# Performance work log

Hardware: AMD Instinct MI355X
Metric: run time of the kernel (lower is better)

The kernel has to match this reference:

```python
import jax, jax.numpy as jnp
import numpy as np

EPS = 1e-6          # module eps for denominator
KERNEL_EPS = 1e-4   # performer softmax_kernel numerical eps


def softmax_kernel(data, projection):
    # data: [n, l, h, e]; projection: [m, e] -> features [n, l, h, m]
    d = data.shape[-1]
    m = projection.shape[0]
    data_normalizer = d ** -0.25
    ratio = m ** -0.5
    data_dash = jnp.einsum('nlhe,me->nlhm', data * data_normalizer, projection)
    diag_data = (0.5 * (data_normalizer ** 2)) * jnp.sum(data * data, axis=-1, keepdims=True)
    # numerically stable exp with per-row max subtraction
    data_dash = ratio * (jnp.exp(data_dash - diag_data - jnp.max(data_dash, axis=-1, keepdims=True)) + KERNEL_EPS)
    return data_dash


def _gaussian_orthogonal_random_matrix(nb_rows, nb_cols, seed=0):
    rng = np.random.default_rng(seed)
    blocks = []
    for _ in range(int(np.ceil(nb_rows / nb_cols))):
        q, _ = np.linalg.qr(rng.standard_normal((nb_cols, nb_cols)))
        blocks.append(q.T)
    proj = np.concatenate(blocks, axis=0)[:nb_rows]
    # scaling=0: chi-distributed row multipliers
    multiplier = np.linalg.norm(rng.standard_normal((nb_rows, nb_cols)), axis=1)
    return (multiplier[:, None] * proj).astype(np.float32)


def setup_inputs() -> dict:
    n, l, h, e = 2, 2048, 8, 64
    nb_features = l  # module: nb_features = l when l >= e
    key = jax.random.key(0)
    kq, kk, kv = jax.random.split(key, 3)
    queries = jax.random.normal(kq, (n, l, h, e), jnp.float32)
    keys = jax.random.normal(kk, (n, l, h, e), jnp.float32)
    values = jax.random.normal(kv, (n, l, h, e), jnp.float32)
    projection = jnp.asarray(_gaussian_orthogonal_random_matrix(nb_features, e))
    return {"queries": queries, "keys": keys, "values": values, "projection": projection}


def reference(queries, keys, values, projection):
    # Performer linear attention, batched (bi=None) branch
    q = softmax_kernel(queries, projection)   # [n, l, h, m]
    k = softmax_kernel(keys, projection)      # [n, l, h, m]
    kv = jnp.einsum('nshm,nshe->nhem', k, values)              # [n, h, e, m]
    z = 1.0 / (jnp.einsum('nlhm,nhm->nlh', q, k.sum(axis=1)) + EPS)  # [n, l, h]
    v = jnp.einsum('nlhm,nhem,nlh->nlhe', q, kv, z)             # [n, l, h, e]
    return v
```

## Files before the change

### kernel.cpp

```cpp
#include <hip/hip_runtime.h>


#define LL 2048
#define HH 8
#define MM 2048
#define ROWSTR 512

#define NORMC 0.35355339059327373f
#define LOG2E 1.4426950408889634f
#define NORMC2 (NORMC * LOG2E)
#define RATIO 0.022097086912079608f
#define KEPS 1e-4f
#define REPS (RATIO * KEPS)
#define EPSD 1e-6f

#define KVSPLIT 2097152
#define RSPLIT 32768

typedef __attribute__((ext_vector_type(8))) short short8;
typedef __attribute__((ext_vector_type(16))) float f32x16;

#define MFMA32(a, b, c) __builtin_amdgcn_mfma_f32_32x32x16_bf16((a), (b), (c), 0, 0, 0)

__device__ __forceinline__ void wg_barrier_lds() {
    asm volatile("s_waitcnt lgkmcnt(0)" ::: "memory");
    __builtin_amdgcn_s_barrier();
    __builtin_amdgcn_sched_barrier(0);
}

__device__ __forceinline__ f32x16 zero16() {
    f32x16 v;
    #pragma unroll
    for (int i = 0; i < 16; ++i) v[i] = 0.f;
    return v;
}
__device__ __forceinline__ unsigned short f2bf(float f) {
    union { float f; unsigned int u; } v; v.f = f;
    unsigned int r = v.u + 0x7fffu + ((v.u >> 16) & 1u);
    return (unsigned short)(r >> 16);
}
__device__ __forceinline__ unsigned int pk2(float lo, float hi) {
    return __builtin_amdgcn_perm(__float_as_uint(hi), __float_as_uint(lo), 0x07060302u);
}
__device__ __forceinline__ float bf2f(unsigned short u) {
    union { unsigned int ui; float f; } v; v.ui = ((unsigned int)u) << 16; return v.f;
}

template <bool BF16>
__device__ __forceinline__ short8 row_load8(const void* src, size_t rowbase, int off) {
    if (BF16) {
        return *(const short8*)((const unsigned short*)src + rowbase + off);
    } else {
        const float* p = (const float*)src + rowbase + off;
        float4 f0 = ((const float4*)p)[0], f1 = ((const float4*)p)[1];
        union { unsigned int u[4]; short8 s; } v;
        v.u[0] = pk2(f0.x, f0.y); v.u[1] = pk2(f0.z, f0.w);
        v.u[2] = pk2(f1.x, f1.y); v.u[3] = pk2(f1.z, f1.w);
        return v.s;
    }
}

template <bool BF16>
__device__ __forceinline__ void tile_load(const void* src, size_t base, size_t rstride,
                                          int t, uint4& A, uint4& B) {
    const int row = t >> 2, c16 = (t & 3) * 16;
    if (BF16) {
        const unsigned short* p = (const unsigned short*)src + base + (size_t)row * rstride + c16;
        A = *(const uint4*)p;
        B = *(const uint4*)(p + 8);
    } else {
        const float* p = (const float*)src + base + (size_t)row * rstride + c16;
        float4 f0 = ((const float4*)p)[0], f1 = ((const float4*)p)[1];
        float4 f2 = ((const float4*)p)[2], f3 = ((const float4*)p)[3];
        A.x = pk2(f0.x, f0.y); A.y = pk2(f0.z, f0.w);
        A.z = pk2(f1.x, f1.y); A.w = pk2(f1.z, f1.w);
        B.x = pk2(f2.x, f2.y); B.y = pk2(f2.z, f2.w);
        B.z = pk2(f3.x, f3.y); B.w = pk2(f3.z, f3.w);
    }
}
__device__ __forceinline__ void tile_store72(unsigned short* D, int t, uint4 A, uint4 B) {
    const int row = t >> 2, c16 = (t & 3) * 16;
    *(uint4*)&D[row * 72 + c16] = A;
    *(uint4*)&D[row * 72 + c16 + 8] = B;
}

template <bool BF16>
__device__ __forceinline__ void vt_load(const void* V, size_t base, int t, uint4& A, uint4& B) {
    const int s0 = (t & 31) * 2, e0 = (t >> 5) * 8;
    if (BF16) {
        const unsigned short* p = (const unsigned short*)V + base + (size_t)s0 * ROWSTR + e0;
        A = *(const uint4*)p;
        B = *(const uint4*)(p + ROWSTR);
    } else {
        const float* p = (const float*)V + base + (size_t)s0 * ROWSTR + e0;
        float4 f0 = ((const float4*)p)[0], f1 = ((const float4*)p)[1];
        const float* q = p + ROWSTR;
        float4 g0 = ((const float4*)q)[0], g1 = ((const float4*)q)[1];
        A.x = pk2(f0.x, f0.y); A.y = pk2(f0.z, f0.w);
        A.z = pk2(f1.x, f1.y); A.w = pk2(f1.z, f1.w);
        B.x = pk2(g0.x, g0.y); B.y = pk2(g0.z, g0.w);
        B.z = pk2(g1.x, g1.y); B.w = pk2(g1.z, g1.w);
    }
}
__device__ __forceinline__ void vt_store72(unsigned short* VT, int t, uint4 A, uint4 B) {
    const int s0 = (t & 31) * 2, e0 = (t >> 5) * 8;
    const unsigned ua[4] = {A.x, A.y, A.z, A.w}, ub[4] = {B.x, B.y, B.z, B.w};
    #pragma unroll
    for (int i = 0; i < 4; ++i) {
        *(unsigned*)&VT[(e0 + 2 * i) * 72 + s0] = (ua[i] & 0xFFFFu) | (ub[i] << 16);
        *(unsigned*)&VT[(e0 + 2 * i + 1) * 72 + s0] = (ua[i] >> 16) | (ub[i] & 0xFFFF0000u);
    }
}

__device__ __forceinline__ short8 xfrag(const unsigned int pd[8], int cp, int hi) {
    const unsigned int s0 = hi ? pd[4 * cp + 0] : pd[4 * cp + 2];
    const unsigned int s1 = hi ? pd[4 * cp + 1] : pd[4 * cp + 3];
    const unsigned int r0 = (unsigned int)__shfl_xor((int)s0, 32);
    const unsigned int r1 = (unsigned int)__shfl_xor((int)s1, 32);
    union { unsigned int u[4]; short8 s; } v;
    v.u[0] = hi ? r0 : pd[4 * cp + 0];
    v.u[1] = hi ? r1 : pd[4 * cp + 1];
    v.u[2] = hi ? pd[4 * cp + 2] : r0;
    v.u[3] = hi ? pd[4 * cp + 3] : r1;
    return v.s;
}

__global__ void LinearAttention_15985868276494_detect(const unsigned short* __restrict__ P,
                                                      float* __restrict__ flag) {
    if (threadIdx.x == 0) {
        int sane = 1;
        #pragma unroll
        for (int i = 0; i < 16; ++i) {
            const unsigned e = (P[2 * i] >> 7) & 0xFF;
            if (e < 101 || e > 141) sane = 0;
        }
        *flag = sane ? 1.0f : 0.0f;
    }
}

template <bool BF16>
__device__ void stats_impl(const void* X, const void* P, float* cws,
                           unsigned short* Ps, float* red) {
    const int t = threadIdx.x;
    const int w = t >> 6, ln = t & 31, hi = (t >> 5) & 1;
    const int mstrip = w & 1, rstrip = w >> 1;
    const int row_base = blockIdx.x * 256;

    short8 xb[4];
    #pragma unroll
    for (int c = 0; c < 4; ++c)
        xb[c] = row_load8<BF16>(X, (size_t)(row_base + rstrip * 32 + ln) * 64, 16 * c + 8 * hi);

    const bool stP = (t < 256);
    const int tl = t & 255;
    uint4 pA, pB;
    if (stP) {
        uint4 a0, b0;
        tile_load<BF16>(P, 0, 64, tl, a0, b0);
        tile_store72(Ps, tl, a0, b0);
        tile_load<BF16>(P, (size_t)64 * 64, 64, tl, pA, pB);
    }
    wg_barrier_lds();

    float rmax = -3e38f;
    for (int i = 0; i < 32; ++i) {
        const int cur = i & 1;
        unsigned short* Pc = Ps + cur * 4608;
        f32x16 acc = zero16();
        #pragma unroll
        for (int c = 0; c < 4; ++c) {
            const short8 af = *(const short8*)&Pc[(32 * mstrip + ln) * 72 + 16 * c + 8 * hi];
            acc = MFMA32(af, xb[c], acc);
        }
        if (stP && i + 1 < 32) {
            tile_store72(Ps + (cur ^ 1) * 4608, tl, pA, pB);
            if (i + 2 < 32)
                tile_load<BF16>(P, (size_t)((i + 2) * 64) * 64, 64, tl, pA, pB);
        }
        #pragma unroll
        for (int r = 0; r < 16; ++r) rmax = fmaxf(rmax, acc[r]);
        wg_barrier_lds();
    }
    rmax = fmaxf(rmax, __shfl_xor(rmax, 32));
    if (hi == 0) red[w * 32 + ln] = rmax;
    float s2 = 0.f;
    if (mstrip == 0) {
        #pragma unroll
        for (int c = 0; c < 4; ++c) {
            union { short8 s; unsigned int u[4]; } uv; uv.s = xb[c];
            #pragma unroll
            for (int i2 = 0; i2 < 4; ++i2) {
                const float lo = bf2f((unsigned short)(uv.u[i2] & 0xFFFF));
                const float hv = bf2f((unsigned short)(uv.u[i2] >> 16));
                s2 = fmaf(lo, lo, s2); s2 = fmaf(hv, hv, s2);
            }
        }
        s2 += __shfl_xor(s2, 32);
    }
    wg_barrier_lds();
    if (mstrip == 0 && hi == 0) {
        const float rm = fmaxf(red[w * 32 + ln], red[(w + 1) * 32 + ln]);
        const int rg = row_base + rstrip * 32 + ln;
        const int n = rg >> 14, l = (rg >> 3) & 2047, h = rg & 7;
        cws[(size_t)((n << 3) | h) * LL + l] =
            (NORMC * rm + (0.5f * NORMC * NORMC) * s2) * LOG2E;
    }
}

__global__ __launch_bounds__(1024, 4) void LinearAttention_15985868276494_stats(
        const void* K, const void* Q, const void* P, const float* flag,
        float* c_k, float* c_q) {
    __shared__ unsigned short Ps[2 * 64 * 72];
    __shared__ float red[512];
    const void* X = (blockIdx.y == 0) ? K : Q;
    float* cws = (blockIdx.y == 0) ? c_k : c_q;
    if (*flag != 0.f) stats_impl<true>(X, P, cws, Ps, red);
    else stats_impl<false>(X, P, cws, Ps, red);
}

template <bool BF16>
__device__ void kv_impl(const void* K, const void* V, const void* P, const float* cws,
                        float* kvf01, float* ksum01, char* smem) {
    unsigned short* Ks = (unsigned short*)smem;
    unsigned short* VT = (unsigned short*)(smem + 18432);
    float* cks = (float*)(smem + 36864);
    float* fin = (float*)smem;

    const int t = threadIdx.x;
    const int w = t >> 6, ln = t & 31, hi = (t >> 5) & 1;
    const int w2 = w & 3, ep = w >> 2;
    const int sstrip = w2 & 1, msub = w2 >> 1;
    const int mc = ep * 2 + msub;
    const int bid = blockIdx.x;
    const int xcd = bid & 7, rr = bid >> 3;
    const int gq = rr >> 3, mtb = rr & 7;
    const int g = gq * 8 + xcd;
    const int nh = g >> 1, sp = g & 1;
    const int n = nh >> 3, h = nh & 7;
    const size_t xbase = (size_t)n * (LL * ROWSTR) + (size_t)h * 64;
    const int st0 = sp * 16;
    const int mbase = mtb * 256;

    const bool stK = (t < 256), stV = (t >= 256 && t < 512);
    const int tl = t & 255;

    short8 pb[4];
    #pragma unroll
    for (int c = 0; c < 4; ++c)
        pb[c] = row_load8<BF16>(P, (size_t)(mbase + mc * 32 + ln) * 64, 16 * c + 8 * hi);

    uint4 kA, kB, vA, vB; float ckr = 0.f;
    if (stK) {
        tile_load<BF16>(K, xbase + (size_t)(st0 * 64) * ROWSTR, ROWSTR, tl, kA, kB);
        tile_store72(Ks, tl, kA, kB);
        tile_load<BF16>(K, xbase + (size_t)((st0 + 1) * 64) * ROWSTR, ROWSTR, tl, kA, kB);
    } else if (stV) {
        vt_load<BF16>(V, xbase + (size_t)(st0 * 64) * ROWSTR, tl, vA, vB);
        vt_store72(VT, tl, vA, vB);
        vt_load<BF16>(V, xbase + (size_t)((st0 + 1) * 64) * ROWSTR, tl, vA, vB);
    }
    if (t < 64) {
        cks[t] = cws[(size_t)nh * LL + st0 * 64 + t];
        ckr = cws[(size_t)nh * LL + (st0 + 1) * 64 + t];
    }
    wg_barrier_lds();

    const short8 ones = {0x3F80, 0x3F80, 0x3F80, 0x3F80, 0x3F80, 0x3F80, 0x3F80, 0x3F80};
    f32x16 akv0 = zero16(), akv1 = zero16(), aks = zero16();

    for (int i = 0; i < 16; ++i) {
        const int cur = i & 1;
        unsigned short* Kc = Ks + cur * 4608;
        unsigned short* Vc = VT + cur * 4608;
        const float* cc = cks + cur * 64;
        f32x16 D = zero16();
        #pragma unroll
        for (int c = 0; c < 4; ++c) {
            const short8 af = *(const short8*)&Kc[(32 * sstrip + ln) * 72 + 16 * c + 8 * hi];
            D = MFMA32(af, pb[c], D);
        }
        if (i + 1 < 16) {
            if (stK) tile_store72(Ks + (cur ^ 1) * 4608, tl, kA, kB);
            else if (stV) vt_store72(VT + (cur ^ 1) * 4608, tl, vA, vB);
            if (t < 64) cks[(cur ^ 1) * 64 + t] = ckr;
            if (i + 2 < 16) {
                const int st = st0 + i + 2;
                if (stK) tile_load<BF16>(K, xbase + (size_t)(st * 64) * ROWSTR, ROWSTR, tl, kA, kB);
                else if (stV) vt_load<BF16>(V, xbase + (size_t)(st * 64) * ROWSTR, tl, vA, vB);
                if (t < 64) ckr = cws[(size_t)nh * LL + st * 64 + t];
            }
        }
        unsigned int pd[8];
        #pragma unroll
        for (int gIdx = 0; gIdx < 4; ++gIdx) {
            const float4 c4 = *(const float4*)&cc[32 * sstrip + 8 * gIdx + 4 * hi];
            const float ca[4] = {c4.x, c4.y, c4.z, c4.w};
            float f[4];
            #pragma unroll
            for (int b = 0; b < 4; ++b) {
                const float arg = fminf(fmaf(D[4 * gIdx + b], NORMC2, -ca[b]), 0.f);
                f[b] = fmaf(__builtin_amdgcn_exp2f(arg), RATIO, REPS);
            }
            pd[2 * gIdx] = pk2(f[0], f[1]);
            pd[2 * gIdx + 1] = pk2(f[2], f[3]);
        }
        #pragma unroll
        for (int cp = 0; cp < 2; ++cp) {
            const short8 bf = xfrag(pd, cp, hi);
            const int scol = 32 * sstrip + 16 * cp + 8 * hi;
            const short8 v0 = *(const short8*)&Vc[ln * 72 + scol];
            const short8 v1 = *(const short8*)&Vc[(32 + ln) * 72 + scol];
            akv0 = MFMA32(v0, bf, akv0);
            akv1 = MFMA32(v1, bf, akv1);
            aks = MFMA32(ones, bf, aks);
        }
        wg_barrier_lds();
    }
    #pragma unroll 1
    for (int e4 = 0; e4 < 4; ++e4) {
        if (ep == e4) {
            const int slot = (w2 * 64 + (t & 63)) * 33;
            #pragma unroll
            for (int r = 0; r < 16; ++r) fin[slot + r] = akv0[r];
            #pragma unroll
            for (int r = 0; r < 16; ++r) fin[slot + 16 + r] = akv1[r];
            fin[slot + 32] = aks[0];
        }
        wg_barrier_lds();
        if (ep == e4) {
            const int tt = t & 255;
            const int mt = mtb * 4 + e4;
            const int e = tt >> 2;
            const int t16 = e >> 5, e5 = e & 31;
            const int hi_s = (e5 >> 2) & 1;
            const int reg = 16 * t16 + (e5 & 3) + 4 * (e5 >> 3);
            float* dst = kvf01 + (size_t)sp * KVSPLIT + (size_t)nh * (64 * MM)
                       + (size_t)e * MM + mt * 64 + (tt & 3) * 16;
            #pragma unroll
            for (int jq = 0; jq < 4; ++jq) {
                float o[4];
                #pragma unroll
                for (int b = 0; b < 4; ++b) {
                    const int m_local = (tt & 3) * 16 + 4 * jq + b;
                    const int ms = m_local >> 5;
                    const int lane_s = hi_s * 32 + (m_local & 31);
                    o[b] = fin[((2 * ms) * 64 + lane_s) * 33 + reg]
                         + fin[((2 * ms + 1) * 64 + lane_s) * 33 + reg];
                }
                *(float4*)&dst[4 * jq] = make_float4(o[0], o[1], o[2], o[3]);
            }
            if (tt < 64) {
                const int ms = tt >> 5;
                const float val = fin[((2 * ms) * 64 + (tt & 31)) * 33 + 32]
                                + fin[((2 * ms + 1) * 64 + (tt & 31)) * 33 + 32];
                ksum01[(size_t)sp * RSPLIT + (size_t)nh * MM + mt * 64 + tt] = val;
            }
        }
        wg_barrier_lds();
    }
}

__global__ __launch_bounds__(1024, 4) void LinearAttention_15985868276494_kv(
        const void* K, const void* V, const void* P, const float* flag,
        const float* cws, float* kvf01, float* ksum01) {
    extern __shared__ char smem_kv[];
    if (*flag != 0.f) kv_impl<true>(K, V, P, cws, kvf01, ksum01, smem_kv);
    else kv_impl<false>(K, V, P, cws, kvf01, ksum01, smem_kv);
}

__global__ __launch_bounds__(256) void LinearAttention_15985868276494_reduce(
        const float* __restrict__ kvf01, const float* __restrict__ ksum01,
        unsigned short* __restrict__ kvT, float* __restrict__ ksumW) {
    const int gid = blockIdx.x * 256 + threadIdx.x;
    const size_t i4 = (size_t)gid * 4;
    const float4 a = *(const float4*)&kvf01[i4];
    const float4 b = *(const float4*)&kvf01[KVSPLIT + i4];
    uint2 o;
    o.x = (unsigned)f2bf(a.x + b.x) | ((unsigned)f2bf(a.y + b.y) << 16);
    o.y = (unsigned)f2bf(a.z + b.z) | ((unsigned)f2bf(a.w + b.w) << 16);
    *(uint2*)&kvT[i4] = o;
    if (blockIdx.x < 32) {
        const float4 c = *(const float4*)&ksum01[i4];
        const float4 d = *(const float4*)&ksum01[RSPLIT + i4];
        *(float4*)&ksumW[i4] = make_float4(c.x + d.x, c.y + d.y, c.z + d.z, c.w + d.w);
    }
}

template <bool BF16>
__device__ void out_impl(const void* Q, const void* P, const float* cqw,
                         const unsigned short* kvT, const float* ksum,
                         float* po, float* pad, char* smem) {
    unsigned short* Ps = (unsigned short*)smem;
    unsigned short* KVs = (unsigned short*)(smem + 18432);
    unsigned short* kss = (unsigned short*)(smem + 36864);
    float* fin = (float*)smem;

    const int t = threadIdx.x;
    const int w = t >> 6, ln = t & 31, hi = (t >> 5) & 1;
    const int w2 = w & 3, ep = w >> 2;
    const int mstrip = w2 & 1, lsub = w2 >> 1;
    const int lc = ep * 2 + lsub;
    const int bid = blockIdx.x;
    const int xcd = bid & 7, rr = bid >> 3;
    const int gq = rr >> 3, lbb = rr & 7;
    const int g = gq * 8 + xcd;
    const int nh = g >> 1, sp = g & 1;
    const int n = nh >> 3, h = nh & 7;
    const size_t qbase = (size_t)n * (LL * ROWSTR) + (size_t)h * 64;
    const size_t kvbase = (size_t)nh * (size_t)(64 * MM);
    const int mt0 = sp * 16;
    const int lbase = lbb * 256;

    const bool stP = (t < 256), stKV = (t >= 256 && t < 512);
    const int tl = t & 255;

    short8 qb[4];
    #pragma unroll
    for (int c = 0; c < 4; ++c)
        qb[c] = row_load8<BF16>(Q, qbase + (size_t)(lbase + lc * 32 + ln) * ROWSTR, 16 * c + 8 * hi);
    const float cq = cqw[(size_t)nh * LL + lbase + lc * 32 + ln];

    uint4 pA, pB, kA, kB; float ksr = 0.f;
    if (stP) {
        tile_load<BF16>(P, (size_t)(mt0 * 64) * 64, 64, tl, pA, pB);
        tile_store72(Ps, tl, pA, pB);
        tile_load<BF16>(P, (size_t)((mt0 + 1) * 64) * 64, 64, tl, pA, pB);
    } else if (stKV) {
        tile_load<true>(kvT, kvbase + mt0 * 64, MM, tl, kA, kB);
        tile_store72(KVs, tl, kA, kB);
        tile_load<true>(kvT, kvbase + (mt0 + 1) * 64, MM, tl, kA, kB);
    }
    if (t < 64) {
        kss[t] = f2bf(ksum[(size_t)nh * MM + mt0 * 64 + t]);
        ksr = ksum[(size_t)nh * MM + (mt0 + 1) * 64 + t];
    }
    wg_barrier_lds();

    f32x16 ao0 = zero16(), ao1 = zero16(), ad = zero16();

    for (int i = 0; i < 16; ++i) {
        const int cur = i & 1;
        unsigned short* Pc = Ps + cur * 4608;
        unsigned short* Kc = KVs + cur * 4608;
        const unsigned short* ksc = kss + cur * 64;
        f32x16 D = zero16();
        #pragma unroll
        for (int c = 0; c < 4; ++c) {
            const short8 af = *(const short8*)&Pc[(32 * mstrip + ln) * 72 + 16 * c + 8 * hi];
            D = MFMA32(af, qb[c], D);
        }
        if (i + 1 < 16) {
            if (stP) tile_store72(Ps + (cur ^ 1) * 4608, tl, pA, pB);
            else if (stKV) tile_store72(KVs + (cur ^ 1) * 4608, tl, kA, kB);
            if (t < 64) kss[(cur ^ 1) * 64 + t] = f2bf(ksr);
            if (i + 2 < 16) {
                if (stP) tile_load<BF16>(P, (size_t)((mt0 + i + 2) * 64) * 64, 64, tl, pA, pB);
                else if (stKV) tile_load<true>(kvT, kvbase + (mt0 + i + 2) * 64, MM, tl, kA, kB);
                if (t < 64) ksr = ksum[(size_t)nh * MM + (mt0 + i + 2) * 64 + t];
            }
        }
        unsigned int pd[8];
        #pragma unroll
        for (int gIdx = 0; gIdx < 4; ++gIdx) {
            float f[4];
            #pragma unroll
            for (int b = 0; b < 4; ++b) {
                const float arg = fminf(fmaf(D[4 * gIdx + b], NORMC2, -cq), 0.f);
                f[b] = fmaf(__builtin_amdgcn_exp2f(arg), RATIO, REPS);
            }
            pd[2 * gIdx] = pk2(f[0], f[1]);
            pd[2 * gIdx + 1] = pk2(f[2], f[3]);
        }
        #pragma unroll
        for (int cp = 0; cp < 2; ++cp) {
            const short8 bf = xfrag(pd, cp, hi);
            const int mcol = 32 * mstrip + 16 * cp + 8 * hi;
            const short8 a0 = *(const short8*)&Kc[ln * 72 + mcol];
            const short8 a1 = *(const short8*)&Kc[(32 + ln) * 72 + mcol];
            const short8 k8 = *(const short8*)&ksc[mcol];
            ao0 = MFMA32(a0, bf, ao0);
            ao1 = MFMA32(a1, bf, ao1);
            ad = MFMA32(k8, bf, ad);
        }
        wg_barrier_lds();
    }
    #pragma unroll 1
    for (int e4 = 0; e4 < 4; ++e4) {
        if (ep == e4) {
            const int slot = (w2 * 64 + (t & 63)) * 33;
            #pragma unroll
            for (int r = 0; r < 16; ++r) fin[slot + r] = ao0[r];
            #pragma unroll
            for (int r = 0; r < 16; ++r) fin[slot + 16 + r] = ao1[r];
            fin[slot + 32] = ad[0];
        }
        wg_barrier_lds();
        if (ep == e4) {
            const int tt = t & 255;
            const int l_local = tt >> 2, eg = tt & 3;
            const int ls = l_local >> 5, lane_l = l_local & 31;
            const float adt = fin[((2 * ls) * 64 + lane_l) * 33 + 32]
                            + fin[((2 * ls + 1) * 64 + lane_l) * 33 + 32];
            const int l = (lbb * 4 + e4) * 64 + l_local;
            const size_t row = (size_t)(n * LL + l) * HH + h;
            if (eg == 0) pad[(size_t)sp * RSPLIT + row] = adt;
            float* dst = po + (size_t)sp * KVSPLIT + row * 64 + eg * 16;
            #pragma unroll
            for (int jq = 0; jq < 4; ++jq) {
                float o[4];
                #pragma unroll
                for (int b = 0; b < 4; ++b) {
                    const int e = eg * 16 + 4 * jq + b;
                    const int t16 = e >> 5, e5 = e & 31;
                    const int hi_s = (e5 >> 2) & 1;
                    const int reg = 16 * t16 + (e5 & 3) + 4 * (e5 >> 3);
                    const int lane_s = hi_s * 32 + lane_l;
                    o[b] = fin[((2 * ls) * 64 + lane_s) * 33 + reg]
                         + fin[((2 * ls + 1) * 64 + lane_s) * 33 + reg];
                }
                *(float4*)&dst[4 * jq] = make_float4(o[0], o[1], o[2], o[3]);
            }
        }
        wg_barrier_lds();
    }
}

__global__ __launch_bounds__(1024, 4) void LinearAttention_15985868276494_out(
        const void* Q, const void* P, const float* flag, const float* cqw,
        const unsigned short* kvT, const float* ksum, float* po, float* pad) {
    extern __shared__ char smem_out[];
    if (*flag != 0.f) out_impl<true>(Q, P, cqw, kvT, ksum, po, pad, smem_out);
    else out_impl<false>(Q, P, cqw, kvT, ksum, po, pad, smem_out);
}

__global__ __launch_bounds__(256) void LinearAttention_15985868276494_out2(
        const float* __restrict__ po, const float* __restrict__ pad,
        const float* __restrict__ flag, void* __restrict__ outp) {
    const int gid = blockIdx.x * 256 + threadIdx.x;
    const int row = gid >> 2, eg = gid & 3;
    const float adt = pad[row] + pad[RSPLIT + row];
    const float z = 1.0f / (adt + EPSD);
    const size_t base = (size_t)row * 64 + eg * 16;
    float vals[16];
    #pragma unroll
    for (int q4 = 0; q4 < 4; ++q4) {
        const float4 a = *(const float4*)&po[base + 4 * q4];
        const float4 b = *(const float4*)&po[KVSPLIT + base + 4 * q4];
        vals[4 * q4 + 0] = (a.x + b.x) * z;
        vals[4 * q4 + 1] = (a.y + b.y) * z;
        vals[4 * q4 + 2] = (a.z + b.z) * z;
        vals[4 * q4 + 3] = (a.w + b.w) * z;
    }
    if (*flag != 0.f) {
        uint4 o0, o1;
        o0.x = (unsigned)f2bf(vals[0]) | ((unsigned)f2bf(vals[1]) << 16);
        o0.y = (unsigned)f2bf(vals[2]) | ((unsigned)f2bf(vals[3]) << 16);
        o0.z = (unsigned)f2bf(vals[4]) | ((unsigned)f2bf(vals[5]) << 16);
        o0.w = (unsigned)f2bf(vals[6]) | ((unsigned)f2bf(vals[7]) << 16);
        o1.x = (unsigned)f2bf(vals[8]) | ((unsigned)f2bf(vals[9]) << 16);
        o1.y = (unsigned)f2bf(vals[10]) | ((unsigned)f2bf(vals[11]) << 16);
        o1.z = (unsigned)f2bf(vals[12]) | ((unsigned)f2bf(vals[13]) << 16);
        o1.w = (unsigned)f2bf(vals[14]) | ((unsigned)f2bf(vals[15]) << 16);
        unsigned short* op = (unsigned short*)outp + base;
        *(uint4*)op = o0;
        *(uint4*)(op + 8) = o1;
    } else {
        float* op = (float*)outp + base;
        #pragma unroll
        for (int q4 = 0; q4 < 4; ++q4)
            *(float4*)&op[4 * q4] = make_float4(vals[4 * q4], vals[4 * q4 + 1],
                                                vals[4 * q4 + 2], vals[4 * q4 + 3]);
    }
}

extern "C" void kernel_launch(void* const* d_in, const int* in_sizes, int n_in,
                              void* d_out, int out_size, void* d_ws, size_t ws_size,
                              hipStream_t stream) {
    const void* Q = d_in[0];
    const void* K = d_in[1];
    const void* V = d_in[2];
    const void* P = d_in[3];

    float* W = (float*)d_ws;
    float* flag = W;
    float* c_k = W + 16;
    float* c_q = c_k + 32768;
    float* ksum01 = c_q + 32768;
    float* kvf01 = ksum01 + 2 * RSPLIT;
    float* ksumW = kvf01 + 2 * KVSPLIT;
    unsigned short* kvTW = (unsigned short*)(ksumW + RSPLIT);

    LinearAttention_15985868276494_detect<<<1, 64, 0, stream>>>(
        (const unsigned short*)P, flag);
    LinearAttention_15985868276494_stats<<<dim3(128, 2), 1024, 0, stream>>>(
        K, Q, P, flag, c_k, c_q);
    LinearAttention_15985868276494_kv<<<dim3(256), 1024, 37376, stream>>>(
        K, V, P, flag, c_k, kvf01, ksum01);
    LinearAttention_15985868276494_reduce<<<2048, 256, 0, stream>>>(
        kvf01, ksum01, kvTW, ksumW);
    LinearAttention_15985868276494_out<<<dim3(256), 1024, 37120, stream>>>(
        Q, P, flag, c_q, kvTW, ksumW, kvf01, ksum01);
    LinearAttention_15985868276494_out2<<<512, 256, 0, stream>>>(
        kvf01, ksum01, flag, d_out);
}
```

Before: 186.1 us.

## Stage multiple tiles per barrier using all threads for LDS staging

After: 190.0 us. 2.1% more time.

```diff
diff --git a/kernel.cpp b/kernel.cpp
--- a/kernel.cpp
+++ b/kernel.cpp
@@ -139,11 +139,13 @@
 }
 
 template <bool BF16>
-__device__ void stats_impl(const void* X, const void* P, float* cws,
-                           unsigned short* Ps, float* red) {
+__device__ void stats_impl(const void* X, const void* P, float* cws, char* smem) {
+    unsigned short* Ps = (unsigned short*)smem;
+    float* red = (float*)(smem + 73728);
     const int t = threadIdx.x;
     const int w = t >> 6, ln = t & 31, hi = (t >> 5) & 1;
     const int mstrip = w & 1, rstrip = w >> 1;
+    const int grp = w >> 2, tl = t & 255;
     const int row_base = blockIdx.x * 256;
 
     short8 xb[4];
@@ -151,34 +153,36 @@
     for (int c = 0; c < 4; ++c)
         xb[c] = row_load8<BF16>(X, (size_t)(row_base + rstrip * 32 + ln) * 64, 16 * c + 8 * hi);
 
-    const bool stP = (t < 256);
-    const int tl = t & 255;
     uint4 pA, pB;
-    if (stP) {
+    {
         uint4 a0, b0;
-        tile_load<BF16>(P, 0, 64, tl, a0, b0);
-        tile_store72(Ps, tl, a0, b0);
-        tile_load<BF16>(P, (size_t)64 * 64, 64, tl, pA, pB);
+        tile_load<BF16>(P, (size_t)(grp * 64) * 64, 64, tl, a0, b0);
+        tile_store72(Ps + grp * 4608, tl, a0, b0);
+        tile_load<BF16>(P, (size_t)((4 + grp) * 64) * 64, 64, tl, pA, pB);
     }
     wg_barrier_lds();
 
     float rmax = -3e38f;
-    for (int i = 0; i < 32; ++i) {
+    for (int i = 0; i < 8; ++i) {
         const int cur = i & 1;
-        unsigned short* Pc = Ps + cur * 4608;
-        f32x16 acc = zero16();
+        unsigned short* Pq = Ps + cur * 18432;
         #pragma unroll
-        for (int c = 0; c < 4; ++c) {
-            const short8 af = *(const short8*)&Pc[(32 * mstrip + ln) * 72 + 16 * c + 8 * hi];
-            acc = MFMA32(af, xb[c], acc);
-        }
-        if (stP && i + 1 < 32) {
-            tile_store72(Ps + (cur ^ 1) * 4608, tl, pA, pB);
-            if (i + 2 < 32)
-                tile_load<BF16>(P, (size_t)((i + 2) * 64) * 64, 64, tl, pA, pB);
-        }
-        #pragma unroll
-        for (int r = 0; r < 16; ++r) rmax = fmaxf(rmax, acc[r]);
+        for (int sub = 0; sub < 4; ++sub) {
+            unsigned short* Pc = Pq + sub * 4608;
+            f32x16 acc = zero16();
+            #pragma unroll
+            for (int c = 0; c < 4; ++c) {
+                const short8 af = *(const short8*)&Pc[(32 * mstrip + ln) * 72 + 16 * c + 8 * hi];
+                acc = MFMA32(af, xb[c], acc);
+            }
+            #pragma unroll
+            for (int r = 0; r < 16; ++r) rmax = fmaxf(rmax, acc[r]);
+            if (sub == 0 && i + 1 < 8) {
+                tile_store72(Ps + (cur ^ 1) * 18432 + grp * 4608, tl, pA, pB);
+                if (i + 2 < 8)
+                    tile_load<BF16>(P, (size_t)(((i + 2) * 4 + grp) * 64) * 64, 64, tl, pA, pB);
+            }
+        }
         wg_barrier_lds();
     }
     rmax = fmaxf(rmax, __shfl_xor(rmax, 32));
@@ -210,20 +214,19 @@
 __global__ __launch_bounds__(1024, 4) void LinearAttention_15985868276494_stats(
         const void* K, const void* Q, const void* P, const float* flag,
         float* c_k, float* c_q) {
-    __shared__ unsigned short Ps[2 * 64 * 72];
-    __shared__ float red[512];
+    extern __shared__ char smem_st[];
     const void* X = (blockIdx.y == 0) ? K : Q;
     float* cws = (blockIdx.y == 0) ? c_k : c_q;
-    if (*flag != 0.f) stats_impl<true>(X, P, cws, Ps, red);
-    else stats_impl<false>(X, P, cws, Ps, red);
+    if (*flag != 0.f) stats_impl<true>(X, P, cws, smem_st);
+    else stats_impl<false>(X, P, cws, smem_st);
 }
 
 template <bool BF16>
 __device__ void kv_impl(const void* K, const void* V, const void* P, const float* cws,
                         float* kvf01, float* ksum01, char* smem) {
     unsigned short* Ks = (unsigned short*)smem;
-    unsigned short* VT = (unsigned short*)(smem + 18432);
-    float* cks = (float*)(smem + 36864);
+    unsigned short* VT = (unsigned short*)(smem + 36864);
+    float* cks = (float*)(smem + 73728);
     float* fin = (float*)smem;
 
     const int t = threadIdx.x;
@@ -231,6 +234,9 @@
     const int w2 = w & 3, ep = w >> 2;
     const int sstrip = w2 & 1, msub = w2 >> 1;
     const int mc = ep * 2 + msub;
+    const int grp = w >> 2, tl = t & 255;
+    const int gsub = grp & 1;
+    const bool isK = (grp < 2);
     const int bid = blockIdx.x;
     const int xcd = bid & 7, rr = bid >> 3;
     const int gq = rr >> 3, mtb = rr & 7;
@@ -241,78 +247,80 @@
     const int st0 = sp * 16;
     const int mbase = mtb * 256;
 
-    const bool stK = (t < 256), stV = (t >= 256 && t < 512);
-    const int tl = t & 255;
-
     short8 pb[4];
     #pragma unroll
     for (int c = 0; c < 4; ++c)
         pb[c] = row_load8<BF16>(P, (size_t)(mbase + mc * 32 + ln) * 64, 16 * c + 8 * hi);
 
     uint4 kA, kB, vA, vB; float ckr = 0.f;
-    if (stK) {
-        tile_load<BF16>(K, xbase + (size_t)(st0 * 64) * ROWSTR, ROWSTR, tl, kA, kB);
-        tile_store72(Ks, tl, kA, kB);
-        tile_load<BF16>(K, xbase + (size_t)((st0 + 1) * 64) * ROWSTR, ROWSTR, tl, kA, kB);
-    } else if (stV) {
-        vt_load<BF16>(V, xbase + (size_t)(st0 * 64) * ROWSTR, tl, vA, vB);
-        vt_store72(VT, tl, vA, vB);
-        vt_load<BF16>(V, xbase + (size_t)((st0 + 1) * 64) * ROWSTR, tl, vA, vB);
-    }
-    if (t < 64) {
+    if (isK) {
+        tile_load<BF16>(K, xbase + (size_t)((st0 + gsub) * 64) * ROWSTR, ROWSTR, tl, kA, kB);
+        tile_store72(Ks + gsub * 4608, tl, kA, kB);
+        tile_load<BF16>(K, xbase + (size_t)((st0 + 2 + gsub) * 64) * ROWSTR, ROWSTR, tl, kA, kB);
+    } else {
+        vt_load<BF16>(V, xbase + (size_t)((st0 + gsub) * 64) * ROWSTR, tl, vA, vB);
+        vt_store72(VT + gsub * 4608, tl, vA, vB);
+        vt_load<BF16>(V, xbase + (size_t)((st0 + 2 + gsub) * 64) * ROWSTR, tl, vA, vB);
+    }
+    if (t < 128) {
         cks[t] = cws[(size_t)nh * LL + st0 * 64 + t];
-        ckr = cws[(size_t)nh * LL + (st0 + 1) * 64 + t];
+        ckr = cws[(size_t)nh * LL + st0 * 64 + 128 + t];
     }
     wg_barrier_lds();
 
     const short8 ones = {0x3F80, 0x3F80, 0x3F80, 0x3F80, 0x3F80, 0x3F80, 0x3F80, 0x3F80};
     f32x16 akv0 = zero16(), akv1 = zero16(), aks = zero16();
 
-    for (int i = 0; i < 16; ++i) {
+    for (int i = 0; i < 8; ++i) {
         const int cur = i & 1;
-        unsigned short* Kc = Ks + cur * 4608;
-        unsigned short* Vc = VT + cur * 4608;
-        const float* cc = cks + cur * 64;
-        f32x16 D = zero16();
+        unsigned short* Kq = Ks + cur * 9216;
+        unsigned short* Vq = VT + cur * 9216;
+        const float* cc = cks + cur * 128;
         #pragma unroll
-        for (int c = 0; c < 4; ++c) {
-            const short8 af = *(const short8*)&Kc[(32 * sstrip + ln) * 72 + 16 * c + 8 * hi];
-            D = MFMA32(af, pb[c], D);
-        }
-        if (i + 1 < 16) {
-            if (stK) tile_store72(Ks + (cur ^ 1) * 4608, tl, kA, kB);
-            else if (stV) vt_store72(VT + (cur ^ 1) * 4608, tl, vA, vB);
-            if (t < 64) cks[(cur ^ 1) * 64 + t] = ckr;
-            if (i + 2 < 16) {
-                const int st = st0 + i + 2;
-                if (stK) tile_load<BF16>(K, xbase + (size_t)(st * 64) * ROWSTR, ROWSTR, tl, kA, kB);
-                else if (stV) vt_load<BF16>(V, xbase + (size_t)(st * 64) * ROWSTR, tl, vA, vB);
-                if (t < 64) ckr = cws[(size_t)nh * LL + st * 64 + t];
-            }
-        }
-        unsigned int pd[8];
-        #pragma unroll
-        for (int gIdx = 0; gIdx < 4; ++gIdx) {
-            const float4 c4 = *(const float4*)&cc[32 * sstrip + 8 * gIdx + 4 * hi];
-            const float ca[4] = {c4.x, c4.y, c4.z, c4.w};
-            float f[4];
-            #pragma unroll
-            for (int b = 0; b < 4; ++b) {
-                const float arg = fminf(fmaf(D[4 * gIdx + b], NORMC2, -ca[b]), 0.f);
-                f[b] = fmaf(__builtin_amdgcn_exp2f(arg), RATIO, REPS);
-            }
-            pd[2 * gIdx] = pk2(f[0], f[1]);
-            pd[2 * gIdx + 1] = pk2(f[2], f[3]);
-        }
-        #pragma unroll
-        for (int cp = 0; cp < 2; ++cp) {
-            const short8 bf = xfrag(pd, cp, hi);
-            const int scol = 32 * sstrip + 16 * cp + 8 * hi;
-            const short8 v0 = *(const short8*)&Vc[ln * 72 + scol];
-            const short8 v1 = *(const short8*)&Vc[(32 + ln) * 72 + scol];
-            akv0 = MFMA32(v0, bf, akv0);
-            akv1 = MFMA32(v1, bf, akv1);
-            aks = MFMA32(ones, bf, aks);
+        for (int sub = 0; sub < 2; ++sub) {
+            unsigned short* Kc = Kq + sub * 4608;
+            unsigned short* Vc = Vq + sub * 4608;
+            f32x16 D = zero16();
+            #pragma unroll
+            for (int c = 0; c < 4; ++c) {
+                const short8 af = *(const short8*)&Kc[(32 * sstrip + ln) * 72 + 16 * c + 8 * hi];
+                D = MFMA32(af, pb[c], D);
+            }
+            if (sub == 0 && i + 1 < 8) {
+                if (isK) tile_store72(Ks + (cur ^ 1) * 9216 + gsub * 4608, tl, kA, kB);
+                else vt_store72(VT + (cur ^ 1) * 9216 + gsub * 4608, tl, vA, vB);
+                if (t < 128) cks[(cur ^ 1) * 128 + t] = ckr;
+                if (i + 2 < 8) {
+                    const int st = st0 + 2 * (i + 2) + gsub;
+                    if (isK) tile_load<BF16>(K, xbase + (size_t)(st * 64) * ROWSTR, ROWSTR, tl, kA, kB);
+                    else vt_load<BF16>(V, xbase + (size_t)(st * 64) * ROWSTR, tl, vA, vB);
+                    if (t < 128) ckr = cws[(size_t)nh * LL + (st0 + 2 * (i + 2)) * 64 + t];
+                }
+            }
+            unsigned int pd[8];
+            #pragma unroll
+            for (int gIdx = 0; gIdx < 4; ++gIdx) {
+                const float4 c4 = *(const float4*)&cc[sub * 64 + 32 * sstrip + 8 * gIdx + 4 * hi];
+                const float ca[4] = {c4.x, c4.y, c4.z, c4.w};
+                float f[4];
+                #pragma unroll
+                for (int b = 0; b < 4; ++b) {
+                    const float arg = fminf(fmaf(D[4 * gIdx + b], NORMC2, -ca[b]), 0.f);
+                    f[b] = fmaf(__builtin_amdgcn_exp2f(arg), RATIO, REPS);
+                }
+                pd[2 * gIdx] = pk2(f[0], f[1]);
+                pd[2 * gIdx + 1] = pk2(f[2], f[3]);
+            }
+            #pragma unroll
+            for (int cp = 0; cp < 2; ++cp) {
+                const short8 bf = xfrag(pd, cp, hi);
+                const int scol = 32 * sstrip + 16 * cp + 8 * hi;
+                const short8 v0 = *(const short8*)&Vc[ln * 72 + scol];
+                const short8 v1 = *(const short8*)&Vc[(32 + ln) * 72 + scol];
+                akv0 = MFMA32(v0, bf, akv0);
+                akv1 = MFMA32(v1, bf, akv1);
+                aks = MFMA32(ones, bf, aks);
+            }
         }
         wg_barrier_lds();
     }
@@ -391,8 +399,8 @@
                          const unsigned short* kvT, const float* ksum,
                          float* po, float* pad, char* smem) {
     unsigned short* Ps = (unsigned short*)smem;
-    unsigned short* KVs = (unsigned short*)(smem + 18432);
-    unsigned short* kss = (unsigned short*)(smem + 36864);
+    unsigned short* KVs = (unsigned short*)(smem + 36864);
+    unsigned short* kss = (unsigned short*)(smem + 73728);
     float* fin = (float*)smem;
 
     const int t = threadIdx.x;
@@ -400,6 +408,9 @@
     const int w2 = w & 3, ep = w >> 2;
     const int mstrip = w2 & 1, lsub = w2 >> 1;
     const int lc = ep * 2 + lsub;
+    const int grp = w >> 2, tl = t & 255;
+    const int gsub = grp & 1;
+    const bool isP = (grp < 2);
     const int bid = blockIdx.x;
     const int xcd = bid & 7, rr = bid >> 3;
     const int gq = rr >> 3, lbb = rr & 7;
@@ -411,9 +422,6 @@
     const int mt0 = sp * 16;
     const int lbase = lbb * 256;
 
-    const bool stP = (t < 256), stKV = (t >= 256 && t < 512);
-    const int tl = t & 255;
-
     short8 qb[4];
     #pragma unroll
     for (int c = 0; c < 4; ++c)
@@ -421,66 +429,72 @@
     const float cq = cqw[(size_t)nh * LL + lbase + lc * 32 + ln];
 
     uint4 pA, pB, kA, kB; float ksr = 0.f;
-    if (stP) {
-        tile_load<BF16>(P, (size_t)(mt0 * 64) * 64, 64, tl, pA, pB);
-        tile_store72(Ps, tl, pA, pB);
-        tile_load<BF16>(P, (size_t)((mt0 + 1) * 64) * 64, 64, tl, pA, pB);
-    } else if (stKV) {
-        tile_load<true>(kvT, kvbase + mt0 * 64, MM, tl, kA, kB);
-        tile_store72(KVs, tl, kA, kB);
-        tile_load<true>(kvT, kvbase + (mt0 + 1) * 64, MM, tl, kA, kB);
-    }
-    if (t < 64) {
+    if (isP) {
+        tile_load<BF16>(P, (size_t)((mt0 + gsub) * 64) * 64, 64, tl, pA, pB);
+        tile_store72(Ps + gsub * 4608, tl, pA, pB);
+        tile_load<BF16>(P, (size_t)((mt0 + 2 + gsub) * 64) * 64, 64, tl, pA, pB);
+    } else {
+        tile_load<true>(kvT, kvbase + (mt0 + gsub) * 64, MM, tl, kA, kB);
+        tile_store72(KVs + gsub * 4608, tl, kA, kB);
+        tile_load<true>(kvT, kvbase + (mt0 + 2 + gsub) * 64, MM, tl, kA, kB);
+    }
+    if (t < 128) {
         kss[t] = f2bf(ksum[(size_t)nh * MM + mt0 * 64 + t]);
-        ksr = ksum[(size_t)nh * MM + (mt0 + 1) * 64 + t];
+        ksr = ksum[(size_t)nh * MM + mt0 * 64 + 128 + t];
     }
     wg_barrier_lds();
 
     f32x16 ao0 = zero16(), ao1 = zero16(), ad = zero16();
 
-    for (int i = 0; i < 16; ++i) {
+    for (int i = 0; i < 8; ++i) {
         const int cur = i & 1;
-        unsigned short* Pc = Ps + cur * 4608;
-        unsigned short* Kc = KVs + cur * 4608;
-        const unsigned short* ksc = kss + cur * 64;
-        f32x16 D = zero16();
+        unsigned short* Pq = Ps + cur * 9216;
+        unsigned short* Kq = KVs + cur * 9216;
+        const unsigned short* ksc = kss + cur * 128;
         #pragma unroll
-        for (int c = 0; c < 4; ++c) {
-            const short8 af = *(const short8*)&Pc[(32 * mstrip + ln) * 72 + 16 * c + 8 * hi];
-            D = MFMA32(af, qb[c], D);
-        }
-        if (i + 1 < 16) {
-            if (stP) tile_store72(Ps + (cur ^ 1) * 4608, tl, pA, pB);
-            else if (stKV) tile_store72(KVs + (cur ^ 1) * 4608, tl, kA, kB);
-            if (t < 64) kss[(cur ^ 1) * 64 + t] = f2bf(ksr);
-            if (i + 2 < 16) {
-                if (stP) tile_load<BF16>(P, (size_t)((mt0 + i + 2) * 64) * 64, 64, tl, pA, pB);
-                else if (stKV) tile_load<true>(kvT, kvbase + (mt0 + i + 2) * 64, MM, tl, kA, kB);
-                if (t < 64) ksr = ksum[(size_t)nh * MM + (mt0 + i + 2) * 64 + t];
-            }
-        }
-        unsigned int pd[8];
-        #pragma unroll
-        for (int gIdx = 0; gIdx < 4; ++gIdx) {
-            float f[4];
-            #pragma unroll
-            for (int b = 0; b < 4; ++b) {
-                const float arg = fminf(fmaf(D[4 * gIdx + b], NORMC2, -cq), 0.f);
-                f[b] = fmaf(__builtin_amdgcn_exp2f(arg), RATIO, REPS);
-            }
-            pd[2 * gIdx] = pk2(f[0], f[1]);
-            pd[2 * gIdx + 1] = pk2(f[2], f[3]);
-        }
-        #pragma unroll
-        for (int cp = 0; cp < 2; ++cp) {
-            const short8 bf = xfrag(pd, cp, hi);
-            const int mcol = 32 * mstrip + 16 * cp + 8 * hi;
-            const short8 a0 = *(const short8*)&Kc[ln * 72 + mcol];
-            const short8 a1 = *(const short8*)&Kc[(32 + ln) * 72 + mcol];
-            const short8 k8 = *(const short8*)&ksc[mcol];
-            ao0 = MFMA32(a0, bf, ao0);
-            ao1 = MFMA32(a1, bf, ao1);
-            ad = MFMA32(k8, bf, ad);
+        for (int sub = 0; sub < 2; ++sub) {
+            unsigned short* Pc = Pq + sub * 4608;
+            unsigned short* Kc = Kq + sub * 4608;
+            f32x16 D = zero16();
+            #pragma unroll
+            for (int c = 0; c < 4; ++c) {
+                const short8 af = *(const short8*)&Pc[(32 * mstrip + ln) * 72 + 16 * c + 8 * hi];
+                D = MFMA32(af, qb[c], D);
+            }
+            if (sub == 0 && i + 1 < 8) {
+                if (isP) tile_store72(Ps + (cur ^ 1) * 9216 + gsub * 4608, tl, pA, pB);
+                else tile_store72(KVs + (cur ^ 1) * 9216 + gsub * 4608, tl, kA, kB);
+                if (t < 128) kss[(cur ^ 1) * 128 + t] = f2bf(ksr);
+                if (i + 2 < 8) {
+                    const int mt = mt0 + 2 * (i + 2) + gsub;
+                    if (isP) tile_load<BF16>(P, (size_t)(mt * 64) * 64, 64, tl, pA, pB);
+                    else tile_load<true>(kvT, kvbase + mt * 64, MM, tl, kA, kB);
+                    if (t < 128) ksr = ksum[(size_t)nh * MM + (mt0 + 2 * (i + 2)) * 64 + t];
+                }
+            }
+            unsigned int pd[8];
+            #pragma unroll
+            for (int gIdx = 0; gIdx < 4; ++gIdx) {
+                float f[4];
+                #pragma unroll
+                for (int b = 0; b < 4; ++b) {
+                    const float arg = fminf(fmaf(D[4 * gIdx + b], NORMC2, -cq), 0.f);
+                    f[b] = fmaf(__builtin_amdgcn_exp2f(arg), RATIO, REPS);
+                }
+                pd[2 * gIdx] = pk2(f[0], f[1]);
+                pd[2 * gIdx + 1] = pk2(f[2], f[3]);
+            }
+            #pragma unroll
+            for (int cp = 0; cp < 2; ++cp) {
+                const short8 bf = xfrag(pd, cp, hi);
+                const int mcol = 32 * mstrip + 16 * cp + 8 * hi;
+                const short8 a0 = *(const short8*)&Kc[ln * 72 + mcol];
+                const short8 a1 = *(const short8*)&Kc[(32 + ln) * 72 + mcol];
+                const short8 k8 = *(const short8*)&ksc[sub * 64 + mcol];
+                ao0 = MFMA32(a0, bf, ao0);
+                ao1 = MFMA32(a1, bf, ao1);
+                ad = MFMA32(k8, bf, ad);
+            }
         }
         wg_barrier_lds();
     }
@@ -592,13 +606,13 @@
 
     LinearAttention_15985868276494_detect<<<1, 64, 0, stream>>>(
         (const unsigned short*)P, flag);
-    LinearAttention_15985868276494_stats<<<dim3(128, 2), 1024, 0, stream>>>(
+    LinearAttention_15985868276494_stats<<<dim3(128, 2), 1024, 75776, stream>>>(
         K, Q, P, flag, c_k, c_q);
-    LinearAttention_15985868276494_kv<<<dim3(256), 1024, 37376, stream>>>(
+    LinearAttention_15985868276494_kv<<<dim3(256), 1024, 74752, stream>>>(
         K, V, P, flag, c_k, kvf01, ksum01);
     LinearAttention_15985868276494_reduce<<<2048, 256, 0, stream>>>(
         kvf01, ksum01, kvTW, ksumW);
-    LinearAttention_15985868276494_out<<<dim3(256), 1024, 37120, stream>>>(
+    LinearAttention_15985868276494_out<<<dim3(256), 1024, 74240, stream>>>(
         Q, P, flag, c_q, kvTW, ksumW, kvf01, ksum01);
     LinearAttention_15985868276494_out2<<<512, 256, 0, stream>>>(
         kvf01, ksum01, flag, d_out);
```

## Software-pipeline projection GEMM with triple buffering and widen stats P tiles

Applied to the files above, without the earlier changes.

After: 217.8 us. 1.17x slower.

```diff
diff --git a/kernel.cpp b/kernel.cpp
--- a/kernel.cpp
+++ b/kernel.cpp
@@ -139,11 +139,13 @@
 }
 
 template <bool BF16>
-__device__ void stats_impl(const void* X, const void* P, float* cws,
-                           unsigned short* Ps, float* red) {
+__device__ void stats_impl(const void* X, const void* P, float* cws, char* smem) {
+    unsigned short* Ps = (unsigned short*)smem;
+    float* red = (float*)(smem + 73728);
     const int t = threadIdx.x;
     const int w = t >> 6, ln = t & 31, hi = (t >> 5) & 1;
     const int mstrip = w & 1, rstrip = w >> 1;
+    const int grp = w >> 2, tl = t & 255;
     const int row_base = blockIdx.x * 256;
 
     short8 xb[4];
@@ -151,34 +153,36 @@
     for (int c = 0; c < 4; ++c)
         xb[c] = row_load8<BF16>(X, (size_t)(row_base + rstrip * 32 + ln) * 64, 16 * c + 8 * hi);
 
-    const bool stP = (t < 256);
-    const int tl = t & 255;
     uint4 pA, pB;
-    if (stP) {
+    {
         uint4 a0, b0;
-        tile_load<BF16>(P, 0, 64, tl, a0, b0);
-        tile_store72(Ps, tl, a0, b0);
-        tile_load<BF16>(P, (size_t)64 * 64, 64, tl, pA, pB);
+        tile_load<BF16>(P, (size_t)(grp * 64) * 64, 64, tl, a0, b0);
+        tile_store72(Ps + grp * 4608, tl, a0, b0);
+        tile_load<BF16>(P, (size_t)((4 + grp) * 64) * 64, 64, tl, pA, pB);
     }
     wg_barrier_lds();
 
     float rmax = -3e38f;
-    for (int i = 0; i < 32; ++i) {
+    for (int i = 0; i < 8; ++i) {
         const int cur = i & 1;
-        unsigned short* Pc = Ps + cur * 4608;
-        f32x16 acc = zero16();
-        #pragma unroll
-        for (int c = 0; c < 4; ++c) {
-            const short8 af = *(const short8*)&Pc[(32 * mstrip + ln) * 72 + 16 * c + 8 * hi];
-            acc = MFMA32(af, xb[c], acc);
-        }
-        if (stP && i + 1 < 32) {
-            tile_store72(Ps + (cur ^ 1) * 4608, tl, pA, pB);
-            if (i + 2 < 32)
-                tile_load<BF16>(P, (size_t)((i + 2) * 64) * 64, 64, tl, pA, pB);
-        }
-        #pragma unroll
-        for (int r = 0; r < 16; ++r) rmax = fmaxf(rmax, acc[r]);
+        unsigned short* Pq = Ps + cur * 18432;
+        #pragma unroll
+        for (int sub = 0; sub < 4; ++sub) {
+            unsigned short* Pc = Pq + sub * 4608;
+            f32x16 acc = zero16();
+            #pragma unroll
+            for (int c = 0; c < 4; ++c) {
+                const short8 af = *(const short8*)&Pc[(32 * mstrip + ln) * 72 + 16 * c + 8 * hi];
+                acc = MFMA32(af, xb[c], acc);
+            }
+            #pragma unroll
+            for (int r = 0; r < 16; ++r) rmax = fmaxf(rmax, acc[r]);
+            if (sub == 0 && i + 1 < 8) {
+                tile_store72(Ps + (cur ^ 1) * 18432 + grp * 4608, tl, pA, pB);
+                if (i + 2 < 8)
+                    tile_load<BF16>(P, (size_t)(((i + 2) * 4 + grp) * 64) * 64, 64, tl, pA, pB);
+            }
+        }
         wg_barrier_lds();
     }
     rmax = fmaxf(rmax, __shfl_xor(rmax, 32));
@@ -210,20 +214,19 @@
 __global__ __launch_bounds__(1024, 4) void LinearAttention_15985868276494_stats(
         const void* K, const void* Q, const void* P, const float* flag,
         float* c_k, float* c_q) {
-    __shared__ unsigned short Ps[2 * 64 * 72];
-    __shared__ float red[512];
+    extern __shared__ char smem_st[];
     const void* X = (blockIdx.y == 0) ? K : Q;
     float* cws = (blockIdx.y == 0) ? c_k : c_q;
-    if (*flag != 0.f) stats_impl<true>(X, P, cws, Ps, red);
-    else stats_impl<false>(X, P, cws, Ps, red);
+    if (*flag != 0.f) stats_impl<true>(X, P, cws, smem_st);
+    else stats_impl<false>(X, P, cws, smem_st);
 }
 
 template <bool BF16>
 __device__ void kv_impl(const void* K, const void* V, const void* P, const float* cws,
                         float* kvf01, float* ksum01, char* smem) {
     unsigned short* Ks = (unsigned short*)smem;
-    unsigned short* VT = (unsigned short*)(smem + 18432);
-    float* cks = (float*)(smem + 36864);
+    unsigned short* VT = (unsigned short*)(smem + 27648);
+    float* cks = (float*)(smem + 46080);
     float* fin = (float*)smem;
 
     const int t = threadIdx.x;
@@ -254,6 +257,8 @@
         tile_load<BF16>(K, xbase + (size_t)(st0 * 64) * ROWSTR, ROWSTR, tl, kA, kB);
         tile_store72(Ks, tl, kA, kB);
         tile_load<BF16>(K, xbase + (size_t)((st0 + 1) * 64) * ROWSTR, ROWSTR, tl, kA, kB);
+        tile_store72(Ks + 4608, tl, kA, kB);
+        tile_load<BF16>(K, xbase + (size_t)((st0 + 2) * 64) * ROWSTR, ROWSTR, tl, kA, kB);
     } else if (stV) {
         vt_load<BF16>(V, xbase + (size_t)(st0 * 64) * ROWSTR, tl, vA, vB);
         vt_store72(VT, tl, vA, vB);
@@ -265,31 +270,40 @@
     }
     wg_barrier_lds();
 
+    f32x16 D = zero16();
+    #pragma unroll
+    for (int c = 0; c < 4; ++c) {
+        const short8 af = *(const short8*)&Ks[(32 * sstrip + ln) * 72 + 16 * c + 8 * hi];
+        D = MFMA32(af, pb[c], D);
+    }
+
     const short8 ones = {0x3F80, 0x3F80, 0x3F80, 0x3F80, 0x3F80, 0x3F80, 0x3F80, 0x3F80};
     f32x16 akv0 = zero16(), akv1 = zero16(), aks = zero16();
 
     for (int i = 0; i < 16; ++i) {
-        const int cur = i & 1;
-        unsigned short* Kc = Ks + cur * 4608;
-        unsigned short* Vc = VT + cur * 4608;
-        const float* cc = cks + cur * 64;
-        f32x16 D = zero16();
-        #pragma unroll
-        for (int c = 0; c < 4; ++c) {
-            const short8 af = *(const short8*)&Kc[(32 * sstrip + ln) * 72 + 16 * c + 8 * hi];
-            D = MFMA32(af, pb[c], D);
-        }
+        f32x16 Dn = zero16();
         if (i + 1 < 16) {
-            if (stK) tile_store72(Ks + (cur ^ 1) * 4608, tl, kA, kB);
-            else if (stV) vt_store72(VT + (cur ^ 1) * 4608, tl, vA, vB);
-            if (t < 64) cks[(cur ^ 1) * 64 + t] = ckr;
-            if (i + 2 < 16) {
-                const int st = st0 + i + 2;
-                if (stK) tile_load<BF16>(K, xbase + (size_t)(st * 64) * ROWSTR, ROWSTR, tl, kA, kB);
-                else if (stV) vt_load<BF16>(V, xbase + (size_t)(st * 64) * ROWSTR, tl, vA, vB);
-                if (t < 64) ckr = cws[(size_t)nh * LL + st * 64 + t];
-            }
-        }
+            unsigned short* Kc = Ks + ((i + 1) % 3) * 4608;
+            #pragma unroll
+            for (int c = 0; c < 4; ++c) {
+                const short8 af = *(const short8*)&Kc[(32 * sstrip + ln) * 72 + 16 * c + 8 * hi];
+                Dn = MFMA32(af, pb[c], Dn);
+            }
+        }
+        if (stK) {
+            if (i + 2 < 16) tile_store72(Ks + ((i + 2) % 3) * 4608, tl, kA, kB);
+            if (i + 3 < 16)
+                tile_load<BF16>(K, xbase + (size_t)((st0 + i + 3) * 64) * ROWSTR, ROWSTR, tl, kA, kB);
+        } else if (stV) {
+            if (i + 1 < 16) vt_store72(VT + ((i + 1) & 1) * 4608, tl, vA, vB);
+            if (i + 2 < 16)
+                vt_load<BF16>(V, xbase + (size_t)((st0 + i + 2) * 64) * ROWSTR, tl, vA, vB);
+        }
+        if (t < 64) {
+            if (i + 1 < 16) cks[((i + 1) & 1) * 64 + t] = ckr;
+            if (i + 2 < 16) ckr = cws[(size_t)nh * LL + (st0 + i + 2) * 64 + t];
+        }
+        const float* cc = cks + (i & 1) * 64;
         unsigned int pd[8];
         #pragma unroll
         for (int gIdx = 0; gIdx < 4; ++gIdx) {
@@ -304,6 +318,7 @@
             pd[2 * gIdx] = pk2(f[0], f[1]);
             pd[2 * gIdx + 1] = pk2(f[2], f[3]);
         }
+        unsigned short* Vc = VT + (i & 1) * 4608;
         #pragma unroll
         for (int cp = 0; cp < 2; ++cp) {
             const short8 bf = xfrag(pd, cp, hi);
@@ -314,6 +329,7 @@
             akv1 = MFMA32(v1, bf, akv1);
             aks = MFMA32(ones, bf, aks);
         }
+        D = Dn;
         wg_barrier_lds();
     }
     #pragma unroll 1
@@ -391,8 +407,8 @@
                          const unsigned short* kvT, const float* ksum,
                          float* po, float* pad, char* smem) {
     unsigned short* Ps = (unsigned short*)smem;
-    unsigned short* KVs = (unsigned short*)(smem + 18432);
-    unsigned short* kss = (unsigned short*)(smem + 36864);
+    unsigned short* KVs = (unsigned short*)(smem + 27648);
+    unsigned short* kss = (unsigned short*)(smem + 46080);
     float* fin = (float*)smem;
 
     const int t = threadIdx.x;
@@ -425,6 +441,8 @@
         tile_load<BF16>(P, (size_t)(mt0 * 64) * 64, 64, tl, pA, pB);
         tile_store72(Ps, tl, pA, pB);
         tile_load<BF16>(P, (size_t)((mt0 + 1) * 64) * 64, 64, tl, pA, pB);
+        tile_store72(Ps + 4608, tl, pA, pB);
+        tile_load<BF16>(P, (size_t)((mt0 + 2) * 64) * 64, 64, tl, pA, pB);
     } else if (stKV) {
         tile_load<true>(kvT, kvbase + mt0 * 64, MM, tl, kA, kB);
         tile_store72(KVs, tl, kA, kB);
@@ -436,28 +454,37 @@
     }
     wg_barrier_lds();
 
+    f32x16 D = zero16();
+    #pragma unroll
+    for (int c = 0; c < 4; ++c) {
+        const short8 af = *(const short8*)&Ps[(32 * mstrip + ln) * 72 + 16 * c + 8 * hi];
+        D = MFMA32(af, qb[c], D);
+    }
+
     f32x16 ao0 = zero16(), ao1 = zero16(), ad = zero16();
 
     for (int i = 0; i < 16; ++i) {
-        const int cur = i & 1;
-        unsigned short* Pc = Ps + cur * 4608;
-        unsigned short* Kc = KVs + cur * 4608;
-        const unsigned short* ksc = kss + cur * 64;
-        f32x16 D = zero16();
-        #pragma unroll
-        for (int c = 0; c < 4; ++c) {
-            const short8 af = *(const short8*)&Pc[(32 * mstrip + ln) * 72 + 16 * c + 8 * hi];
-            D = MFMA32(af, qb[c], D);
-        }
+        f32x16 Dn = zero16();
         if (i + 1 < 16) {
-            if (stP) tile_store72(Ps + (cur ^ 1) * 4608, tl, pA, pB);
-            else if (stKV) tile_store72(KVs + (cur ^ 1) * 4608, tl, kA, kB);
-            if (t < 64) kss[(cur ^ 1) * 64 + t] = f2bf(ksr);
-            if (i + 2 < 16) {
-                if (stP) tile_load<BF16>(P, (size_t)((mt0 + i + 2) * 64) * 64, 64, tl, pA, pB);
-                else if (stKV) tile_load<true>(kvT, kvbase + (mt0 + i + 2) * 64, MM, tl, kA, kB);
-                if (t < 64) ksr = ksum[(size_t)nh * MM + (mt0 + i + 2) * 64 + t];
-            }
+            unsigned short* Pc = Ps + ((i + 1) % 3) * 4608;
+            #pragma unroll
+            for (int c = 0; c < 4; ++c) {
+                const short8 af = *(const short8*)&Pc[(32 * mstrip + ln) * 72 + 16 * c + 8 * hi];
+                Dn = MFMA32(af, qb[c], Dn);
+            }
+        }
+        if (stP) {
+            if (i + 2 < 16) tile_store72(Ps + ((i + 2) % 3) * 4608, tl, pA, pB);
+            if (i + 3 < 16)
+                tile_load<BF16>(P, (size_t)((mt0 + i + 3) * 64) * 64, 64, tl, pA, pB);
+        } else if (stKV) {
+            if (i + 1 < 16) tile_store72(KVs + ((i + 1) & 1) * 4608, tl, kA, kB);
+            if (i + 2 < 16)
+                tile_load<true>(kvT, kvbase + (mt0 + i + 2) * 64, MM, tl, kA, kB);
+        }
+        if (t < 64) {
+            if (i + 1 < 16) kss[((i + 1) & 1) * 64 + t] = f2bf(ksr);
+            if (i + 2 < 16) ksr = ksum[(size_t)nh * MM + (mt0 + i + 2) * 64 + t];
         }
         unsigned int pd[8];
         #pragma unroll
@@ -471,6 +498,8 @@
             pd[2 * gIdx] = pk2(f[0], f[1]);
             pd[2 * gIdx + 1] = pk2(f[2], f[3]);
         }
+        unsigned short* Kc = KVs + (i & 1) * 4608;
+        const unsigned short* ksc = kss + (i & 1) * 64;
         #pragma unroll
         for (int cp = 0; cp < 2; ++cp) {
             const short8 bf = xfrag(pd, cp, hi);
@@ -482,6 +511,7 @@
             ao1 = MFMA32(a1, bf, ao1);
             ad = MFMA32(k8, bf, ad);
         }
+        D = Dn;
         wg_barrier_lds();
     }
     #pragma unroll 1
@@ -592,13 +622,13 @@
 
     LinearAttention_15985868276494_detect<<<1, 64, 0, stream>>>(
         (const unsigned short*)P, flag);
-    LinearAttention_15985868276494_stats<<<dim3(128, 2), 1024, 0, stream>>>(
+    LinearAttention_15985868276494_stats<<<dim3(128, 2), 1024, 75776, stream>>>(
         K, Q, P, flag, c_k, c_q);
-    LinearAttention_15985868276494_kv<<<dim3(256), 1024, 37376, stream>>>(
+    LinearAttention_15985868276494_kv<<<dim3(256), 1024, 46592, stream>>>(
         K, V, P, flag, c_k, kvf01, ksum01);
     LinearAttention_15985868276494_reduce<<<2048, 256, 0, stream>>>(
         kvf01, ksum01, kvTW, ksumW);
-    LinearAttention_15985868276494_out<<<dim3(256), 1024, 37120, stream>>>(
+    LinearAttention_15985868276494_out<<<dim3(256), 1024, 46336, stream>>>(
         Q, P, flag, c_q, kvTW, ksumW, kvf01, ksum01);
     LinearAttention_15985868276494_out2<<<512, 256, 0, stream>>>(
         kvf01, ksum01, flag, d_out);
```
